# Kernel tuning notes

Hardware: AMD Instinct MI355X
Metric: run time of the kernel (lower is better)

The kernel has to match this reference:

```python
import jax, jax.numpy as jnp
import numpy as np

DT_REF = 1.0
EPS = 1e-5

def _ln(x, g, b):
    m = x.mean(-1, keepdims=True)
    v = ((x - m) ** 2).mean(-1, keepdims=True)
    return (x - m) * jax.lax.rsqrt(v + EPS) * g + b

def _conv(x, w):
    return jax.lax.conv_general_dilated(x, w, (1, 1), 'SAME', dimension_numbers=('NCHW', 'OIHW', 'NCHW'))

def _linscan(A, X):
    # h_t = A_t * h_{t-1} + X_t  via associative scan along axis=1 (time)
    def comb(c1, c2):
        a1, x1 = c1
        a2, x2 = c2
        return a1 * a2, x2 + a2 * x1
    return jax.lax.associative_scan(comb, (A, X), axis=1)[1]

def _forward(x_re, x_im, h_re, h_im, flux_re, flux_im, dt, gs_g, gs_b, wc_re, wc_im, bc_re, bc_im, metric, gt_g, gt_b, E_re, E_im, Einv_re, Einv_im, lam_flux, inj_re, inj_im, Wsrc_re, Wsrc_im, Wgate, bgate, lam_re, lam_im, Wg, W1, b1, W2, b2):
    B, T, D, H, W = x_re.shape
    x = jax.lax.complex(x_re, x_im)
    # ---- spatial: LayerNorm + Clifford (complex) conv scaled by Riemannian metric, residual ----
    xf = x.reshape(B * T, D, H, W)
    xr = jnp.concatenate([xf.real, xf.imag], axis=1)  # (N,2D,H,W)
    xn = _ln(xr.transpose(0, 2, 3, 1), gs_g, gs_b).transpose(0, 3, 1, 2)
    nr, ni = jnp.split(xn, 2, axis=1)
    o_re = (_conv(nr, wc_re) - _conv(ni, wc_im)) * metric + bc_re[None, :, None, None]
    o_im = (_conv(nr, wc_im) + _conv(ni, wc_re)) * metric + bc_im[None, :, None, None]
    x = (xf + jax.lax.complex(o_re, o_im)).reshape(B, T, D, H, W)
    # ---- eigenbasis encode ----
    E = jax.lax.complex(E_re, E_im)
    x_eigen = jnp.einsum('btdhw,de->bthwe', x, E)  # (B,T,H,W,D)
    x_mean = x_eigen.mean(axis=(2, 3))  # (B,T,D)
    dt_exp = jnp.broadcast_to(dt[None, :], (B, T))
    # ---- flux tracker: linear recurrence over T via pscan + carry-in correction ----
    A_flux = jnp.exp(-jax.nn.softplus(lam_flux)[None, None] * dt_exp[..., None] / DT_REF)  # (B,T,D) real
    X_flux = x_mean * jax.lax.complex(inj_re, inj_im)[None, None]
    flux_seq = _linscan(A_flux.astype(X_flux.dtype), X_flux)
    decay_cum = jnp.cumprod(A_flux, axis=1)
    flux_seq = flux_seq + jax.lax.complex(flux_re, flux_im)[:, None] * decay_cum
    source = jnp.einsum('btd,de->bte', flux_seq, jax.lax.complex(Wsrc_re, Wsrc_im))
    gate = jax.nn.sigmoid(flux_seq.real @ Wgate + bgate)  # (B,T,D) real in (0,1)
    g = gate[:, :, None, None, :]
    forcing = x_eigen * g + source[:, :, None, None, :] * (1.0 - g)
    # ---- ZOH transition operators ----
    lam = jax.lax.complex(-jax.nn.softplus(lam_re), lam_im)  # (D,) stable eigenvalues
    op_decay = jnp.exp(lam[None, None] * dt_exp[..., None])  # (B,T,D) complex
    op_forcing = (op_decay - 1.0) / lam
    u_t = forcing * op_forcing[:, :, None, None, :]
    h_prev = jax.lax.complex(h_re, h_im).reshape(B, H, W, D)
    u_t = u_t.at[:, 0].add(h_prev * op_decay[:, 0][:, None, None, :])
    A_full = jnp.broadcast_to(op_decay[:, :, None, None, :], u_t.shape)
    u_out = _linscan(A_full, u_t)  # state scan over T, independent per (b,h,w)
    # ---- decode + temporal LayerNorm + soft-MoE FFN residual ----
    x_dec = jnp.einsum('bthwe,ed->btdhw', u_out, jax.lax.complex(Einv_re, Einv_im))
    xr2 = jnp.concatenate([x_dec.real, x_dec.imag], axis=2).reshape(B * T, 2 * D, H, W)
    xn2 = _ln(xr2.transpose(0, 2, 3, 1), gt_g, gt_b)  # (N,H,W,2D)
    gates = jax.nn.softmax(xn2 @ Wg, axis=-1)  # (N,H,W,E)
    delta = jnp.zeros_like(xn2)
    for e in range(Wg.shape[-1]):  # small fixed expert count
        hdn = jax.nn.gelu(xn2 @ W1[e] + b1[e])
        delta = delta + gates[..., e:e + 1] * (hdn @ W2[e] + b2[e])
    y = xn2 + delta
    y_re, y_im = jnp.split(y, 2, axis=-1)
    x_out = jax.lax.complex(y_re, y_im).transpose(0, 3, 1, 2).reshape(B, T, D, H, W)
    z = x + x_out
    return jnp.concatenate([z.real, z.imag], axis=2)  # (B,T,2D,H,W) real view of complex out

def setup_inputs():
    B, T, D, H, W, E, F = 2, 16, 64, 48, 48, 4, 256
    key = jax.random.key(0)
    ks = jax.random.split(key, 32)
    n = lambda i, shape, s=1.0: jax.random.normal(ks[i], shape, dtype=jnp.float32) * s
    return {
        'x_re': n(0, (B, T, D, H, W)), 'x_im': n(1, (B, T, D, H, W)),
        'h_re': n(2, (B * H * W, 1, D)), 'h_im': n(3, (B * H * W, 1, D)),
        'flux_re': n(4, (B, D)), 'flux_im': n(5, (B, D)),
        'dt': jax.random.uniform(ks[6], (T,), dtype=jnp.float32, minval=0.1, maxval=1.0),
        'gs_g': jnp.ones((2 * D,), jnp.float32), 'gs_b': jnp.zeros((2 * D,), jnp.float32),
        'wc_re': n(7, (D, D, 3, 3), 0.02), 'wc_im': n(8, (D, D, 3, 3), 0.02),
        'bc_re': jnp.zeros((D,), jnp.float32), 'bc_im': jnp.zeros((D,), jnp.float32),
        'metric': jnp.ones((H, W), jnp.float32) + n(9, (H, W), 0.01),
        'gt_g': jnp.ones((2 * D,), jnp.float32), 'gt_b': jnp.zeros((2 * D,), jnp.float32),
        'E_re': n(10, (D, D), 0.125), 'E_im': n(11, (D, D), 0.125),
        'Einv_re': n(12, (D, D), 0.125), 'Einv_im': n(13, (D, D), 0.125),
        'lam_flux': n(14, (D,), 0.5),
        'inj_re': n(15, (D,), 0.1), 'inj_im': n(16, (D,), 0.1),
        'Wsrc_re': n(17, (D, D), 0.125), 'Wsrc_im': n(18, (D, D), 0.125),
        'Wgate': n(19, (D, D), 0.125), 'bgate': jnp.zeros((D,), jnp.float32),
        'lam_re': n(20, (D,), 0.5), 'lam_im': n(21, (D,), 0.5),
        'Wg': n(22, (2 * D, E), 0.1),
        'W1': n(23, (E, 2 * D, F), 0.06), 'b1': jnp.zeros((E, F), jnp.float32),
        'W2': n(24, (E, F, 2 * D), 0.04), 'b2': jnp.zeros((E, 2 * D), jnp.float32),
    }

def reference(x_re, x_im, h_re, h_im, flux_re, flux_im, dt, gs_g, gs_b, wc_re, wc_im, bc_re, bc_im, metric, gt_g, gt_b, E_re, E_im, Einv_re, Einv_im, lam_flux, inj_re, inj_im, Wsrc_re, Wsrc_im, Wgate, bgate, lam_re, lam_im, Wg, W1, b1, W2, b2):
    return _forward(x_re, x_im, h_re, h_im, flux_re, flux_im, dt, gs_g, gs_b, wc_re, wc_im, bc_re, bc_im, metric, gt_g, gt_b, E_re, E_im, Einv_re, Einv_im, lam_flux, inj_re, inj_im, Wsrc_re, Wsrc_im, Wgate, bgate, lam_re, lam_im, Wg, W1, b1, W2, b2)
```

## Files before the change

### kernel.cpp

```cpp
#include <hip/hip_runtime.h>
#include <hip/hip_bf16.h>
#include <math.h>

#define NBT 32
#define BB 2
#define TT 16
#define DD 64
#define CC 128
#define HH 48
#define WW2 48
#define HW 2304
#define NEXP 4
#define FF 256
#define EPS 1e-5f
#define PADROWS 2432

typedef __attribute__((ext_vector_type(8))) short bf16x8;
typedef __attribute__((ext_vector_type(4))) float f32x4;
typedef __attribute__((ext_vector_type(4))) unsigned int uint4v;
typedef __attribute__((ext_vector_type(2))) unsigned int uint2v;

static __device__ __forceinline__ unsigned short f2bf(float v) {
  __hip_bfloat16 h = __float2bfloat16(v);
  return *(unsigned short*)&h;
}

#define GLOAD_LDS16(gsrc, ldst) \
  __builtin_amdgcn_global_load_lds((const __attribute__((address_space(1))) unsigned int*)(gsrc), \
                                   (__attribute__((address_space(3))) unsigned int*)(ldst), 16, 0, 0)

__global__ void k_prep(unsigned int* __restrict__ xnb_u, float* __restrict__ xm,
                       const float* __restrict__ wc_re, const float* __restrict__ wc_im,
                       unsigned short* __restrict__ Wt,
                       const float* __restrict__ W1, const float* __restrict__ W2,
                       unsigned short* __restrict__ W1t, unsigned short* __restrict__ W2t,
                       const float* __restrict__ Einv_re, const float* __restrict__ Einv_im,
                       unsigned short* __restrict__ Bdt) {
  int blk = blockIdx.x;
  if (blk < 1024) {
    int u = blk * 256 + threadIdx.x;
    if (u < 4096) xm[u] = 0.f;
    if (u >= 32 * 128 * 64) return;
    int img = u >> 13;
    int rem = u & 8191;
    int row = rem >> 6;
    int cu  = rem & 63;
    int prow = row < 64 ? row : row + 2304;
    xnb_u[((size_t)img * PADROWS + prow) * 64 + cu] = 0u;
  } else if (blk < 1600) {
    int idx = (blk - 1024) * 256 + threadIdx.x;
    int tap = idx / 16384;
    int rem = idx & 16383;
    int cout = rem >> 7, cin = rem & 127;
    float v;
    if (cout < 64) {
      if (cin < 64) v =  wc_re[((size_t)cout * 64 + cin) * 9 + tap];
      else          v = -wc_im[((size_t)cout * 64 + (cin - 64)) * 9 + tap];
    } else {
      int o = cout - 64;
      if (cin < 64) v =  wc_im[((size_t)o * 64 + cin) * 9 + tap];
      else          v =  wc_re[((size_t)o * 64 + (cin - 64)) * 9 + tap];
    }
    Wt[idx] = f2bf(v);
  } else if (blk < 2112) {
    int idx = (blk - 1600) * 256 + threadIdx.x;
    {
      int e = idx >> 15, rem = idx & 32767, j = rem >> 7, k = rem & 127;
      float v = W1[((size_t)e * 128 + k) * 256 + j];
      int sw = ((((k >> 3) ^ (j & 7)) << 3) | (k & 7));
      W1t[(size_t)e * 32768 + j * 128 + sw] = f2bf(v);
    }
    {
      int e = idx >> 15, rem = idx & 32767, c = rem >> 8, k2 = rem & 255;
      float v = W2[((size_t)e * 256 + k2) * 128 + c];
      int sw = ((((k2 >> 3) ^ (c & 7)) << 3) | (k2 & 7));
      W2t[(size_t)e * 32768 + c * 256 + sw] = f2bf(v);
    }
  } else {
    int idx = (blk - 2112) * 256 + threadIdx.x;
    int j = idx >> 7, k = idx & 127;
    float v;
    if (j < 64) {
      if (k < 64) v =  Einv_re[k * 64 + j];
      else        v = -Einv_im[(k - 64) * 64 + j];
    } else {
      int d = j - 64;
      if (k < 64) v =  Einv_im[k * 64 + d];
      else        v =  Einv_re[(k - 64) * 64 + d];
    }
    int sw = ((((k >> 3) ^ (j & 7)) << 3) | (k & 7));
    Bdt[j * 128 + sw] = f2bf(v);
  }
}

__global__ void k_ln1(const float* __restrict__ x_re, const float* __restrict__ x_im,
                      const float* __restrict__ g, const float* __restrict__ b,
                      unsigned short* __restrict__ xnb) {
  int n = blockIdx.x / 36;
  int hw0 = (blockIdx.x % 36) * 64;
  __shared__ float ls[64][129];
  __shared__ float part_s[4][64], part_q[4][64];
  __shared__ float mean_s[64], rstd_s[64];
  int tid = threadIdx.x;
  for (int i = tid; i < 64 * 128; i += 256) {
    int d = i >> 6, p = i & 63;
    float v = (d < DD) ? x_re[((size_t)n * DD + d) * HW + hw0 + p]
                       : x_im[((size_t)n * DD + (d - DD)) * HW + hw0 + p];
    ls[p][d] = v;
  }
  __syncthreads();
  {
    int p = tid & 63, q = tid >> 6;
    float s = 0.f, ss = 0.f;
    for (int c = q * 32; c < q * 32 + 32; c++) { float v = ls[p][c]; s += v; ss += v * v; }
    part_s[q][p] = s; part_q[q][p] = ss;
  }
  __syncthreads();
  if (tid < 64) {
    float s = part_s[0][tid] + part_s[1][tid] + part_s[2][tid] + part_s[3][tid];
    float ss = part_q[0][tid] + part_q[1][tid] + part_q[2][tid] + part_q[3][tid];
    float m = s * (1.f / CC);
    float var = ss * (1.f / CC) - m * m;
    mean_s[tid] = m; rstd_s[tid] = rsqrtf(var + EPS);
  }
  __syncthreads();
  for (int i = tid; i < 64 * 128; i += 256) {
    int p = i >> 7, c = i & 127;
    float v = (ls[p][c] - mean_s[p]) * rstd_s[p] * g[c] + b[c];
    xnb[(((size_t)n * PADROWS) + 64 + hw0 + p) * 128 + c] = f2bf(v);
  }
}

#define TM 128
#define AROWS 226

__global__ __launch_bounds__(512, 1) void k_conv(
    const unsigned short* __restrict__ xnb,
    const unsigned short* __restrict__ Wt,
    const float* __restrict__ bc_re, const float* __restrict__ bc_im,
    const float* __restrict__ metric,
    const float* __restrict__ x_re, const float* __restrict__ x_im,
    float* __restrict__ xp) {
  __shared__ unsigned short As[AROWS * 128];
  __shared__ unsigned short Bs[2][128 * 128];
  int n = blockIdx.x / 18;
  int tile = blockIdx.x % 18;
  int hw0 = tile * TM;
  int tid = threadIdx.x;
  int lane = tid & 63, wv = tid >> 6;
  int wvp = wv >> 1, wvc = wv & 1;
  int r16 = lane & 15, kgrp = lane >> 4;

  const unsigned short* xbase = xnb + ((size_t)n * PADROWS + 64 + hw0 - 49) * 128;
  for (int i = tid; i < AROWS * 16; i += 512) {
    int row = i >> 4, ch = i & 15;
    GLOAD_LDS16(xbase + (size_t)row * 128 + ((ch ^ (row & 7)) << 3), &As[i * 8]);
  }
  {
    #pragma unroll
    for (int it = 0; it < 4; it++) {
      int i = it * 512 + tid;
      int row = i >> 4, ch = i & 15;
      GLOAD_LDS16(Wt + (size_t)row * 128 + ((ch ^ (row & 7)) << 3), &Bs[0][i * 8]);
    }
  }

  f32x4 acc[2][4];
  #pragma unroll
  for (int am = 0; am < 2; am++)
    #pragma unroll
    for (int n0 = 0; n0 < 4; n0++) acc[am][n0] = (f32x4){0.f, 0.f, 0.f, 0.f};

  int w0 = (hw0 + wvp * 32 + r16) % 48;
  int w1 = (hw0 + wvp * 32 + 16 + r16) % 48;

  __syncthreads();

  for (int tap = 0; tap < 9; tap++) {
    int cur = tap & 1;
    if (tap < 8) {
      const unsigned short* wbase = Wt + (size_t)(tap + 1) * 16384;
      #pragma unroll
      for (int it = 0; it < 4; it++) {
        int i = it * 512 + tid;
        int row = i >> 4, ch = i & 15;
        GLOAD_LDS16(wbase + (size_t)row * 128 + ((ch ^ (row & 7)) << 3), &Bs[cur ^ 1][i * 8]);
      }
    }
    int ky = tap / 3, kx = tap % 3;
    int delta = (ky - 1) * 48 + (kx - 1);
    bool v0 = (unsigned)(w0 + kx - 1) < 48u;
    bool v1 = (unsigned)(w1 + kx - 1) < 48u;
    int lp0 = wvp * 32 + r16 + delta + 49;
    int lp1 = lp0 + 16;
    __builtin_amdgcn_s_setprio(1);
    #pragma unroll
    for (int k0 = 0; k0 < 4; k0++) {
      bf16x8 a0 = {0,0,0,0,0,0,0,0}, a1 = {0,0,0,0,0,0,0,0};
      if (v0) a0 = *(const bf16x8*)(As + lp0 * 128 + (((k0 * 4 + kgrp) ^ (lp0 & 7)) << 3));
      if (v1) a1 = *(const bf16x8*)(As + lp1 * 128 + (((k0 * 4 + kgrp) ^ (lp1 & 7)) << 3));
      #pragma unroll
      for (int n0 = 0; n0 < 4; n0++) {
        int brow = wvc * 64 + n0 * 16 + r16;
        bf16x8 b = *(const bf16x8*)(&Bs[cur][brow * 128 + (((k0 * 4 + kgrp) ^ (brow & 7)) << 3)]);
        acc[0][n0] = __builtin_amdgcn_mfma_f32_16x16x32_bf16(a0, b, acc[0][n0], 0, 0, 0);
        acc[1][n0] = __builtin_amdgcn_mfma_f32_16x16x32_bf16(a1, b, acc[1][n0], 0, 0, 0);
      }
    }
    __builtin_amdgcn_s_setprio(0);
    __syncthreads();
  }

  #pragma unroll
  for (int am = 0; am < 2; am++) {
    int prow0 = wvp * 32 + am * 16 + kgrp * 4;
    int pix0 = hw0 + prow0;
    f32x4 mets = *(const f32x4*)(metric + pix0);
    #pragma unroll
    for (int n0 = 0; n0 < 4; n0++) {
      int col = wvc * 64 + n0 * 16 + r16;
      float bias = (col < DD) ? bc_re[col] : bc_im[col - DD];
      const float* xsrc = (col < DD) ? (x_re + ((size_t)n * DD + col) * HW)
                                     : (x_im + ((size_t)n * DD + (col - DD)) * HW);
      f32x4 xres = *(const f32x4*)(xsrc + pix0);
      #pragma unroll
      for (int j = 0; j < 4; j++) {
        float v = acc[am][n0][j] * mets[j] + bias + xres[j];
        xp[((size_t)n * HW + pix0 + j) * 128 + col] = v;
      }
    }
  }
}

__global__ __launch_bounds__(256, 2) void k_eigen(
    const float* __restrict__ xp,
    const float* __restrict__ E_re, const float* __restrict__ E_im,
    float* __restrict__ eg_re, float* __restrict__ eg_im,
    float* __restrict__ xm_re, float* __restrict__ xm_im) {
  __shared__ float Xs[64 * 128];
  __shared__ float Ers[4096], Eis[4096];
  int tid = threadIdx.x;
  int pos0 = blockIdx.x * 64;
  int n = blockIdx.x / 36;
  for (int i = tid; i < 4096; i += 256) { Ers[i] = E_re[i]; Eis[i] = E_im[i]; }
  const float* xb = xp + (size_t)pos0 * 128;
  #pragma unroll
  for (int it = 0; it < 8; it++) {
    int ci = it * 256 + tid;
    int p = ci >> 5, c4 = ci & 31;
    f32x4 v = *(const f32x4*)(xb + (size_t)ci * 4);
    *(f32x4*)&Xs[p * 128 + ((c4 ^ (p & 7)) << 2)] = v;
  }
  __syncthreads();
  int egq = tid & 15, pg = tid >> 4;
  int e0 = egq * 4, swz = pg & 7;
  f32x4 acr[4], aci[4];
  #pragma unroll
  for (int i = 0; i < 4; i++) { acr[i] = (f32x4){0.f,0.f,0.f,0.f}; aci[i] = (f32x4){0.f,0.f,0.f,0.f}; }
  for (int d4 = 0; d4 < 16; d4++) {
    f32x4 xr[4], xi[4];
    #pragma unroll
    for (int i = 0; i < 4; i++) {
      int p = pg + 16 * i;
      xr[i] = *(const f32x4*)&Xs[p * 128 + ((d4 ^ swz) << 2)];
      xi[i] = *(const f32x4*)&Xs[p * 128 + (((d4 + 16) ^ swz) << 2)];
    }
    #pragma unroll
    for (int j = 0; j < 4; j++) {
      int d = d4 * 4 + j;
      f32x4 er = *(const f32x4*)&Ers[d * 64 + e0];
      f32x4 ei = *(const f32x4*)&Eis[d * 64 + e0];
      #pragma unroll
      for (int i = 0; i < 4; i++) {
        acr[i] += xr[i][j] * er - xi[i][j] * ei;
        aci[i] += xr[i][j] * ei + xi[i][j] * er;
      }
    }
  }
  #pragma unroll
  for (int i = 0; i < 4; i++) {
    size_t p = (size_t)(pos0 + pg + 16 * i);
    *(f32x4*)&eg_re[p * 64 + e0] = acr[i];
    *(f32x4*)&eg_im[p * 64 + e0] = aci[i];
  }
  __syncthreads();
  float* red = (float*)Xs;
  f32x4 psr = acr[0] + acr[1] + acr[2] + acr[3];
  f32x4 psi = aci[0] + aci[1] + aci[2] + aci[3];
  *(f32x4*)&red[pg * 64 + e0] = psr;
  *(f32x4*)&red[1024 + pg * 64 + e0] = psi;
  __syncthreads();
  if (tid < 128) {
    int e = tid & 63, which = tid >> 6;
    const float* rb = red + which * 1024;
    float s = 0.f;
    #pragma unroll
    for (int p = 0; p < 16; p++) s += rb[p * 64 + e];
    float* dst = which ? xm_im : xm_re;
    atomicAdd(&dst[n * DD + e], s * (1.f / HW));
  }
}

__global__ void k_seq1(const float* __restrict__ xm_re, const float* __restrict__ xm_im,
                       const float* __restrict__ dt, const float* __restrict__ lam_flux,
                       const float* __restrict__ inj_re, const float* __restrict__ inj_im,
                       const float* __restrict__ flux_re0, const float* __restrict__ flux_im0,
                       float* __restrict__ frg, float* __restrict__ fig) {
  int b = blockIdx.x;
  int e = threadIdx.x;
  float lx = lam_flux[e];
  float sp = lx > 20.f ? lx : log1pf(expf(lx));
  float f_r = flux_re0[b * DD + e], f_i = flux_im0[b * DD + e];
  float ij_r = inj_re[e], ij_i = inj_im[e];
  for (int t = 0; t < TT; t++) {
    float A = expf(-sp * dt[t]);
    int bt = b * TT + t;
    float xr = xm_re[bt * DD + e], xi = xm_im[bt * DD + e];
    f_r = A * f_r + (xr * ij_r - xi * ij_i);
    f_i = A * f_i + (xr * ij_i + xi * ij_r);
    frg[bt * DD + e] = f_r; fig[bt * DD + e] = f_i;
  }
}

__global__ void k_seq2(const float* __restrict__ frg, const float* __restrict__ fig,
                       const float* __restrict__ dt,
                       const float* __restrict__ Wsrc_re, const float* __restrict__ Wsrc_im,
                       const float* __restrict__ Wgate, const float* __restrict__ bgate,
                       const float* __restrict__ lam_re, const float* __restrict__ lam_im,
                       float* __restrict__ gate, float* __restrict__ src_re, float* __restrict__ src_im,
                       float* __restrict__ od_re, float* __restrict__ od_im,
                       float* __restrict__ of_re, float* __restrict__ of_im) {
  int bt = blockIdx.x;
  int t = bt % TT;
  int e = threadIdx.x;
  __shared__ float fr[DD], fi[DD];
  fr[e] = frg[bt * DD + e];
  fi[e] = fig[bt * DD + e];
  __syncthreads();
  float sr = 0.f, si = 0.f, gl = bgate[e];
  for (int d2 = 0; d2 < DD; d2++) {
    float r = fr[d2], im = fi[d2];
    float wr = Wsrc_re[d2 * DD + e], wi = Wsrc_im[d2 * DD + e];
    sr += r * wr - im * wi;
    si += r * wi + im * wr;
    gl += r * Wgate[d2 * DD + e];
  }
  src_re[bt * DD + e] = sr; src_im[bt * DD + e] = si;
  gate[bt * DD + e] = 1.f / (1.f + expf(-gl));
  float lre = lam_re[e];
  float lr_v = -(lre > 20.f ? lre : log1pf(expf(lre)));
  float li_v = lam_im[e];
  float den = lr_v * lr_v + li_v * li_v;
  float dtv = dt[t];
  float mag = expf(lr_v * dtv);
  float odr = mag * cosf(li_v * dtv);
  float odi = mag * sinf(li_v * dtv);
  od_re[bt * DD + e] = odr; od_im[bt * DD + e] = odi;
  of_re[bt * DD + e] = ((odr - 1.f) * lr_v + odi * li_v) / den;
  of_im[bt * DD + e] = (odi * lr_v - (odr - 1.f) * li_v) / den;
}

__global__ void k_uscan(float* __restrict__ eg_re, float* __restrict__ eg_im,
                        const float* __restrict__ gate,
                        const float* __restrict__ src_re, const float* __restrict__ src_im,
                        const float* __restrict__ od_re, const float* __restrict__ od_im,
                        const float* __restrict__ of_re, const float* __restrict__ of_im,
                        const float* __restrict__ h_re, const float* __restrict__ h_im) {
  size_t gid = (size_t)blockIdx.x * 256 + threadIdx.x;
  int e = (int)(gid & 63);
  size_t rem = gid >> 6;
  int hw = (int)(rem % HW);
  int b = (int)(rem / HW);
  float u_r = 0.f, u_i = 0.f;
  for (int t = 0; t < TT; t++) {
    int bt = b * TT + t;
    size_t idx = ((size_t)bt * HW + hw) * DD + e;
    float g = gate[bt * DD + e];
    float fr2 = eg_re[idx] * g + src_re[bt * DD + e] * (1.f - g);
    float fi2 = eg_im[idx] * g + src_im[bt * DD + e] * (1.f - g);
    float ofr = of_re[bt * DD + e], ofi = of_im[bt * DD + e];
    float ut_r = fr2 * ofr - fi2 * ofi;
    float ut_i = fr2 * ofi + fi2 * ofr;
    float odr = od_re[bt * DD + e], odi = od_im[bt * DD + e];
    if (t == 0) {
      size_t hidx = ((size_t)b * HW + hw) * DD + e;
      float hr = h_re[hidx], hi = h_im[hidx];
      ut_r += hr * odr - hi * odi;
      ut_i += hr * odi + hi * odr;
    }
    float nu_r = odr * u_r - odi * u_i + ut_r;
    float nu_i = odr * u_i + odi * u_r + ut_i;
    u_r = nu_r; u_i = nu_i;
    eg_re[idx] = u_r; eg_im[idx] = u_i;
  }
}

__global__ __launch_bounds__(256, 2) void k_dmoe(
    const float* u_re, const float* u_im,
    const unsigned short* __restrict__ Bdt,
    const float* __restrict__ Wg,
    float* __restrict__ gates,
    const float* __restrict__ xp,
    const unsigned short* __restrict__ W1t, const unsigned short* __restrict__ W2t,
    const float* __restrict__ b1, const float* __restrict__ b2,
    const float* __restrict__ gt_g, const float* __restrict__ gt_b,
    float* __restrict__ out) {
  __shared__ __attribute__((aligned(16))) unsigned char smem[81920];
  int tid = threadIdx.x;
  int blk = blockIdx.x;
  int n = blk / 36;
  int hw0 = (blk % 36) * 64;
  size_t pos0 = (size_t)blk * 64;
  int lane = tid & 63, w = tid >> 6, wm = w >> 1, wn = w & 1;
  int r16 = lane & 15, kgrp = lane >> 4;

  {
    unsigned short* BdL = (unsigned short*)smem;
    unsigned short* Au  = (unsigned short*)(smem + 32768);
    #pragma unroll
    for (int it = 0; it < 8; it++)
      GLOAD_LDS16(Bdt + (size_t)(it * 256 + tid) * 8, &BdL[(it * 256 + tid) * 8]);
    #pragma unroll
    for (int it = 0; it < 8; it++) {
      int ci = it * 256 + tid;
      int p = ci >> 5, c4 = ci & 31;
      f32x4 v;
      if (c4 < 16) v = *(const f32x4*)(u_re + (size_t)(pos0 + p) * 64 + c4 * 4);
      else         v = *(const f32x4*)(u_im + (size_t)(pos0 + p) * 64 + (c4 - 16) * 4);
      unsigned int lo = (unsigned int)f2bf(v[0]) | ((unsigned int)f2bf(v[1]) << 16);
      unsigned int hi = (unsigned int)f2bf(v[2]) | ((unsigned int)f2bf(v[3]) << 16);
      int chunk = c4 >> 1, sub = (c4 & 1) * 4;
      *(uint2v*)&Au[p * 128 + ((chunk ^ (p & 7)) << 3) + sub] = (uint2v){lo, hi};
    }
    __syncthreads();
    f32x4 accD[2][4];
    #pragma unroll
    for (int mt = 0; mt < 2; mt++)
      #pragma unroll
      for (int nt = 0; nt < 4; nt++) accD[mt][nt] = (f32x4){0.f, 0.f, 0.f, 0.f};
    #pragma unroll
    for (int ks = 0; ks < 4; ks++) {
      int kc = ks * 4 + kgrp;
      bf16x8 a[2], bb[4];
      #pragma unroll
      for (int mt = 0; mt < 2; mt++) {
        int r = wm * 32 + mt * 16 + r16;
        a[mt] = *(const bf16x8*)&Au[r * 128 + ((kc ^ (r & 7)) << 3)];
      }
      #pragma unroll
      for (int nt = 0; nt < 4; nt++) {
        int j = wn * 64 + nt * 16 + r16;
        bb[nt] = *(const bf16x8*)&BdL[j * 128 + ((kc ^ (j & 7)) << 3)];
      }
      #pragma unroll
      for (int mt = 0; mt < 2; mt++)
        #pragma unroll
        for (int nt = 0; nt < 4; nt++)
          accD[mt][nt] = __builtin_amdgcn_mfma_f32_16x16x32_bf16(a[mt], bb[nt], accD[mt][nt], 0, 0, 0);
    }
    __syncthreads();
    float* DsD = (float*)smem;
    #pragma unroll
    for (int mt = 0; mt < 2; mt++) {
      int row0 = wm * 32 + mt * 16 + kgrp * 4;
      #pragma unroll
      for (int nt = 0; nt < 4; nt++) {
        int c = wn * 64 + nt * 16 + r16;
        #pragma unroll
        for (int jj = 0; jj < 4; jj++)
          DsD[(row0 + jj) * 128 + c] = accD[mt][nt][jj];
      }
    }
    __syncthreads();
    float* Yl = (float*)(smem + 32768);
    unsigned short* Xb = (unsigned short*)(smem + 65536);
    int egq = tid & 15, pg = tid >> 4;
    int d0 = egq * 4, swz = pg & 7;
    f32x4 gg0 = *(const f32x4*)(gt_g + d0);
    f32x4 gb0 = *(const f32x4*)(gt_b + d0);
    f32x4 gg1 = *(const f32x4*)(gt_g + 64 + d0);
    f32x4 gb1 = *(const f32x4*)(gt_b + 64 + d0);
    f32x4 wgr[4], wgi[4];
    #pragma unroll
    for (int j = 0; j < 4; j++) {
      wgr[j] = *(const f32x4*)&Wg[(d0 + j) * 4];
      wgi[j] = *(const f32x4*)&Wg[(64 + d0 + j) * 4];
    }
    int cre = ((d0 >> 3) ^ swz) << 3;
    int cim = (((64 + d0) >> 3) ^ swz) << 3;
    int off47 = d0 & 7;
    #pragma unroll
    for (int i = 0; i < 4; i++) {
      int p = pg + 16 * i;
      size_t pos = pos0 + p;
      f32x4 acr = *(const f32x4*)&DsD[p * 128 + d0];
      f32x4 aci = *(const f32x4*)&DsD[p * 128 + 64 + d0];
      float s = acr[0] + acr[1] + acr[2] + acr[3]
              + aci[0] + aci[1] + aci[2] + aci[3];
      float q = acr[0]*acr[0] + acr[1]*acr[1] + acr[2]*acr[2] + acr[3]*acr[3]
              + aci[0]*aci[0] + aci[1]*aci[1] + aci[2]*aci[2] + aci[3]*aci[3];
      #pragma unroll
      for (int off = 8; off >= 1; off >>= 1) {
        s += __shfl_xor(s, off);
        q += __shfl_xor(q, off);
      }
      float mean = s * (1.f / CC);
      float rstd = rsqrtf(q * (1.f / CC) - mean * mean + EPS);
      f32x4 lnr = (acr - mean) * rstd * gg0 + gb0;
      f32x4 lni = (aci - mean) * rstd * gg1 + gb1;
      *(f32x4*)&Yl[p * 128 + d0] = lnr;
      *(f32x4*)&Yl[p * 128 + 64 + d0] = lni;
      f32x4 p4 = lnr[0]*wgr[0] + lnr[1]*wgr[1] + lnr[2]*wgr[2] + lnr[3]*wgr[3]
               + lni[0]*wgi[0] + lni[1]*wgi[1] + lni[2]*wgi[2] + lni[3]*wgi[3];
      float p0 = p4[0], p1 = p4[1], p2 = p4[2], p3 = p4[3];
      #pragma unroll
      for (int off = 8; off >= 1; off >>= 1) {
        p0 += __shfl_xor(p0, off); p1 += __shfl_xor(p1, off);
        p2 += __shfl_xor(p2, off); p3 += __shfl_xor(p3, off);
      }
      if (egq == 0) {
        float m = fmaxf(fmaxf(p0, p1), fmaxf(p2, p3));
        float e0v = __expf(p0 - m), e1v = __expf(p1 - m), e2v = __expf(p2 - m), e3v = __expf(p3 - m);
        float inv = 1.f / (e0v + e1v + e2v + e3v);
        f32x4 g4 = {e0v * inv, e1v * inv, e2v * inv, e3v * inv};
        *(f32x4*)(gates + pos * 4) = g4;
      }
      unsigned int r0 = (unsigned int)f2bf(lnr[0]) | ((unsigned int)f2bf(lnr[1]) << 16);
      unsigned int r1 = (unsigned int)f2bf(lnr[2]) | ((unsigned int)f2bf(lnr[3]) << 16);
      unsigned int i0 = (unsigned int)f2bf(lni[0]) | ((unsigned int)f2bf(lni[1]) << 16);
      unsigned int i1 = (unsigned int)f2bf(lni[2]) | ((unsigned int)f2bf(lni[3]) << 16);
      *(uint2v*)&Xb[p * 128 + cre + off47] = (uint2v){r0, r1};
      *(uint2v*)&Xb[p * 128 + cim + off47] = (uint2v){i0, i1};
    }
  }
  __syncthreads();

  unsigned short* W1s = (unsigned short*)smem;
  unsigned short* W2s = (unsigned short*)(smem + 32768);
  unsigned short* Hs  = (unsigned short*)(smem + 65536);
  float* Ds = (float*)smem;
  f32x4 acc2[2][4];
  {
    const float* YlF = (const float*)(smem + 32768);
    #pragma unroll
    for (int mt = 0; mt < 2; mt++) {
      int row0 = wm * 32 + mt * 16 + kgrp * 4;
      #pragma unroll
      for (int nt = 0; nt < 4; nt++) {
        int c = wn * 64 + nt * 16 + r16;
        #pragma unroll
        for (int jj = 0; jj < 4; jj++)
          acc2[mt][nt][jj] = YlF[(row0 + jj) * 128 + c];
      }
    }
  }
  bf16x8 xa[2][4];
  {
    const unsigned short* Xb = (const unsigned short*)(smem + 65536);
    #pragma unroll
    for (int pt = 0; pt < 2; pt++) {
      int r = wm * 32 + pt * 16 + r16;
      #pragma unroll
      for (int ks = 0; ks < 4; ks++) {
        int kc = ks * 4 + kgrp;
        xa[pt][ks] = *(const bf16x8*)&Xb[r * 128 + ((kc ^ (r & 7)) << 3)];
      }
    }
  }
  __syncthreads();
  {
    #pragma unroll
    for (int it = 0; it < 8; it++)
      GLOAD_LDS16(W1t + (size_t)(it * 256 + tid) * 8, &W1s[(it * 256 + tid) * 8]);
  }
  __syncthreads();

  const float c1 = -2.3022084f;
  const float c2 = -0.10294372f;

  for (int s = 0; s < 8; s++) {
    int e = s >> 1, h = s & 1;
    float grp[2];
    #pragma unroll
    for (int pt = 0; pt < 2; pt++)
      grp[pt] = gates[(pos0 + wm * 32 + pt * 16 + r16) * 4 + e];
    f32x4 b1p[4];
    #pragma unroll
    for (int ft = 0; ft < 4; ft++)
      b1p[ft] = *(const f32x4*)&b1[e * 256 + h * 128 + wn * 64 + ft * 16 + kgrp * 4];
    {
      const unsigned short* w2src = W2t + (size_t)e * 32768 + (size_t)h * 128;
      #pragma unroll
      for (int it = 0; it < 8; it++) {
        int i = it * 256 + tid;
        int c = i >> 4, j = i & 15;
        GLOAD_LDS16(w2src + (size_t)c * 256 + j * 8, &W2s[i * 8]);
      }
    }
    f32x4 acc1[4][2];
    #pragma unroll
    for (int ft = 0; ft < 4; ft++)
      #pragma unroll
      for (int pt = 0; pt < 2; pt++) acc1[ft][pt] = (f32x4){0.f, 0.f, 0.f, 0.f};
    __builtin_amdgcn_s_setprio(1);
    #pragma unroll
    for (int ks = 0; ks < 4; ks++) {
      int kc = ks * 4 + kgrp;
      bf16x8 wf[4];
      #pragma unroll
      for (int ft = 0; ft < 4; ft++) {
        int fr = wn * 64 + ft * 16 + r16;
        wf[ft] = *(const bf16x8*)&W1s[fr * 128 + ((kc ^ (fr & 7)) << 3)];
      }
      #pragma unroll
      for (int ft = 0; ft < 4; ft++)
        #pragma unroll
        for (int pt = 0; pt < 2; pt++)
          acc1[ft][pt] = __builtin_amdgcn_mfma_f32_16x16x32_bf16(wf[ft], xa[pt][ks], acc1[ft][pt], 0, 0, 0);
    }
    __builtin_amdgcn_s_setprio(0);
    #pragma unroll
    for (int ft = 0; ft < 4; ft++) {
      int f0 = wn * 64 + ft * 16 + kgrp * 4;
      int chunk = f0 >> 3, sub = f0 & 7;
      #pragma unroll
      for (int pt = 0; pt < 2; pt++) {
        int pl = wm * 32 + pt * 16 + r16;
        float gr = grp[pt];
        unsigned short hb[4];
        #pragma unroll
        for (int jj = 0; jj < 4; jj++) {
          float x = acc1[ft][pt][jj] + b1p[ft][jj];
          float z = x * (c1 + c2 * x * x);
          float t = __builtin_amdgcn_exp2f(z);
          hb[jj] = f2bf(x * gr * __builtin_amdgcn_rcpf(1.f + t));
        }
        unsigned int lo = (unsigned int)hb[0] | ((unsigned int)hb[1] << 16);
        unsigned int hi = (unsigned int)hb[2] | ((unsigned int)hb[3] << 16);
        *(uint2v*)&Hs[pl * 128 + ((chunk ^ (pl & 7)) << 3) + sub] = (uint2v){lo, hi};
      }
    }
    __syncthreads();
    if (s < 7) {
      int sn = s + 1;
      const unsigned short* w1src = W1t + (size_t)(sn >> 1) * 32768 + (size_t)(sn & 1) * 16384;
      #pragma unroll
      for (int it = 0; it < 8; it++)
        GLOAD_LDS16(w1src + (size_t)(it * 256 + tid) * 8, &W1s[(it * 256 + tid) * 8]);
    }
    __builtin_amdgcn_s_setprio(1);
    #pragma unroll
    for (int ks = 0; ks < 4; ks++) {
      int kc = ks * 4 + kgrp;
      bf16x8 a[2], bb[4];
      #pragma unroll
      for (int mt = 0; mt < 2; mt++) {
        int r = wm * 32 + mt * 16 + r16;
        a[mt] = *(const bf16x8*)&Hs[r * 128 + ((kc ^ (r & 7)) << 3)];
      }
      #pragma unroll
      for (int nt = 0; nt < 4; nt++) {
        int c = wn * 64 + nt * 16 + r16;
        bb[nt] = *(const bf16x8*)&W2s[c * 128 + ((kc ^ (c & 7)) << 3)];
      }
      #pragma unroll
      for (int mt = 0; mt < 2; mt++)
        #pragma unroll
        for (int nt = 0; nt < 4; nt++)
          acc2[mt][nt] = __builtin_amdgcn_mfma_f32_16x16x32_bf16(a[mt], bb[nt], acc2[mt][nt], 0, 0, 0);
    }
    __builtin_amdgcn_s_setprio(0);
    __syncthreads();
  }

  #pragma unroll
  for (int mt = 0; mt < 2; mt++) {
    int row0 = wm * 32 + mt * 16 + kgrp * 4;
    #pragma unroll
    for (int nt = 0; nt < 4; nt++) {
      int c = wn * 64 + nt * 16 + r16;
      #pragma unroll
      for (int jj = 0; jj < 4; jj++)
        Ds[(row0 + jj) * 129 + c] = acc2[mt][nt][jj];
    }
  }
  __syncthreads();
  #pragma unroll
  for (int it = 0; it < 8; it++) {
    int qi = it * 256 + tid;
    int p = qi >> 5, cq = (qi & 31) << 2;
    size_t pos = pos0 + p;
    f32x4 xpv = *(const f32x4*)&xp[pos * 128 + cq];
    f32x4 g4  = *(const f32x4*)&gates[pos * 4];
    f32x4 bt0 = *(const f32x4*)&b2[0 * CC + cq];
    f32x4 bt1 = *(const f32x4*)&b2[1 * CC + cq];
    f32x4 bt2 = *(const f32x4*)&b2[2 * CC + cq];
    f32x4 bt3 = *(const f32x4*)&b2[3 * CC + cq];
    int base = p * 129 + cq;
    #pragma unroll
    for (int j = 0; j < 4; j++) {
      float bterm = g4[0] * bt0[j] + g4[1] * bt1[j] + g4[2] * bt2[j] + g4[3] * bt3[j];
      Ds[base + j] = xpv[j] + Ds[base + j] + bterm;
    }
  }
  __syncthreads();
  {
    int p = tid & 63;
    int cg = tid >> 6;
    const float* Drow = Ds + p * 129;
    size_t obase = ((size_t)n * CC) * HW + hw0 + p;
    #pragma unroll
    for (int i = 0; i < 32; i++) {
      int c = i * 4 + cg;
      out[obase + (size_t)c * HW] = Drow[c];
    }
  }
}

extern "C" void kernel_launch(void* const* d_in, const int* in_sizes, int n_in,
                              void* d_out, int out_size, void* d_ws, size_t ws_size,
                              hipStream_t stream) {
  const float* x_re   = (const float*)d_in[0];
  const float* x_im   = (const float*)d_in[1];
  const float* h_re   = (const float*)d_in[2];
  const float* h_im   = (const float*)d_in[3];
  const float* flux_re= (const float*)d_in[4];
  const float* flux_im= (const float*)d_in[5];
  const float* dt     = (const float*)d_in[6];
  const float* gs_g   = (const float*)d_in[7];
  const float* gs_b   = (const float*)d_in[8];
  const float* wc_re  = (const float*)d_in[9];
  const float* wc_im  = (const float*)d_in[10];
  const float* bc_re  = (const float*)d_in[11];
  const float* bc_im  = (const float*)d_in[12];
  const float* metric = (const float*)d_in[13];
  const float* gt_g   = (const float*)d_in[14];
  const float* gt_b   = (const float*)d_in[15];
  const float* E_re   = (const float*)d_in[16];
  const float* E_im   = (const float*)d_in[17];
  const float* Einv_re= (const float*)d_in[18];
  const float* Einv_im= (const float*)d_in[19];
  const float* lam_flux=(const float*)d_in[20];
  const float* inj_re = (const float*)d_in[21];
  const float* inj_im = (const float*)d_in[22];
  const float* Wsrc_re= (const float*)d_in[23];
  const float* Wsrc_im= (const float*)d_in[24];
  const float* Wgate  = (const float*)d_in[25];
  const float* bgate  = (const float*)d_in[26];
  const float* lam_re = (const float*)d_in[27];
  const float* lam_im = (const float*)d_in[28];
  const float* Wg     = (const float*)d_in[29];
  const float* W1     = (const float*)d_in[30];
  const float* b1     = (const float*)d_in[31];
  const float* W2     = (const float*)d_in[32];
  const float* b2     = (const float*)d_in[33];

  float* ws = (float*)d_ws;
  const size_t SZ_FULL = (size_t)NBT * HW * CC;
  const size_t SZ_HALF = (size_t)NBT * HW * DD;
  float* xp    = ws;
  float* eg_re = xp + SZ_FULL;
  float* eg_im = eg_re + SZ_HALF;
  float* xr2   = eg_im + SZ_HALF;
  unsigned short* xnb = (unsigned short*)xr2;
  unsigned short* Wt  = (unsigned short*)(xr2 + 5000000);
  float* smalls = xr2 + SZ_FULL;
  float* xm_re = smalls;
  float* xm_im = xm_re + 2048;
  float* gatep = xm_im + 2048;
  float* src_re= gatep + 2048;
  float* src_im= src_re + 2048;
  float* od_re = src_im + 2048;
  float* od_im = od_re + 2048;
  float* of_re = od_im + 2048;
  float* of_im = of_re + 2048;
  float* gates = of_im + 2048;
  unsigned short* W1t = (unsigned short*)(gates + (size_t)NBT * HW * 4);
  unsigned short* W2t = W1t + 131072;
  float* frg = (float*)(W2t + 131072);
  float* fig = frg + 2048;
  unsigned short* Bdt = (unsigned short*)(fig + 2048);

  hipLaunchKernelGGL(k_prep, dim3(2176), dim3(256), 0, stream,
                     (unsigned int*)xnb, xm_re, wc_re, wc_im, Wt, W1, W2, W1t, W2t,
                     Einv_re, Einv_im, Bdt);
  hipLaunchKernelGGL(k_ln1, dim3(NBT * 36), dim3(256), 0, stream, x_re, x_im, gs_g, gs_b, xnb);
  hipLaunchKernelGGL(k_conv, dim3(NBT * 18), dim3(512), 0, stream,
                     xnb, Wt, bc_re, bc_im, metric, x_re, x_im, xp);
  hipLaunchKernelGGL(k_eigen, dim3(1152), dim3(256), 0, stream,
                     xp, E_re, E_im, eg_re, eg_im, xm_re, xm_im);
  hipLaunchKernelGGL(k_seq1, dim3(BB), dim3(DD), 0, stream,
                     xm_re, xm_im, dt, lam_flux, inj_re, inj_im, flux_re, flux_im, frg, fig);
  hipLaunchKernelGGL(k_seq2, dim3(NBT), dim3(DD), 0, stream,
                     frg, fig, dt, Wsrc_re, Wsrc_im, Wgate, bgate, lam_re, lam_im,
                     gatep, src_re, src_im, od_re, od_im, of_re, of_im);
  hipLaunchKernelGGL(k_uscan, dim3(1152), dim3(256), 0, stream,
                     eg_re, eg_im, gatep, src_re, src_im, od_re, od_im, of_re, of_im, h_re, h_im);
  hipLaunchKernelGGL(k_dmoe, dim3(1152), dim3(256), 0, stream,
                     eg_re, eg_im, Bdt, Wg,
                     gates, xp, W1t, W2t, b1, b2, gt_g, gt_b,
                     (float*)d_out);
}
```

Before: 228.5 us.

## Compute eigenbasis projection with bf16 MFMA using a pre-packed complex weight matrix

The complex einsum in k_eigen moves from fp32 scalar FMAs to bf16 MFMA 16x16x32. k_prep gains a block range that packs E_re/E_im into a swizzled 128x128 real-block bf16 matrix, which k_eigen loads into LDS with global_load_lds. The xp tile is converted to bf16 before the multiply. Results are staged through LDS for the stores and the mean reduction. This cuts ALU time in the kernel but lowers the eigen projection to bf16 precision and enlarges the shared-memory footprint.

```diff
diff --git a/kernel.cpp b/kernel.cpp
--- a/kernel.cpp
+++ b/kernel.cpp
@@ -35,7 +35,9 @@
                        const float* __restrict__ W1, const float* __restrict__ W2,
                        unsigned short* __restrict__ W1t, unsigned short* __restrict__ W2t,
                        const float* __restrict__ Einv_re, const float* __restrict__ Einv_im,
-                       unsigned short* __restrict__ Bdt) {
+                       unsigned short* __restrict__ Bdt,
+                       const float* __restrict__ E_re, const float* __restrict__ E_im,
+                       unsigned short* __restrict__ Bet) {
   int blk = blockIdx.x;
   if (blk < 1024) {
     int u = blk * 256 + threadIdx.x;
@@ -76,7 +78,7 @@
       int sw = ((((k2 >> 3) ^ (c & 7)) << 3) | (k2 & 7));
       W2t[(size_t)e * 32768 + c * 256 + sw] = f2bf(v);
     }
-  } else {
+  } else if (blk < 2176) {
     int idx = (blk - 2112) * 256 + threadIdx.x;
     int j = idx >> 7, k = idx & 127;
     float v;
@@ -90,6 +92,20 @@
     }
     int sw = ((((k >> 3) ^ (j & 7)) << 3) | (k & 7));
     Bdt[j * 128 + sw] = f2bf(v);
+  } else {
+    int idx = (blk - 2176) * 256 + threadIdx.x;
+    int j = idx >> 7, k = idx & 127;
+    float v;
+    if (j < 64) {
+      if (k < 64) v =  E_re[k * 64 + j];
+      else        v = -E_im[(k - 64) * 64 + j];
+    } else {
+      int d = j - 64;
+      if (k < 64) v =  E_im[k * 64 + d];
+      else        v =  E_re[(k - 64) * 64 + d];
+    }
+    int sw = ((((k >> 3) ^ (j & 7)) << 3) | (k & 7));
+    Bet[j * 128 + sw] = f2bf(v);
   }
 }
 
@@ -234,59 +250,86 @@
 
 __global__ __launch_bounds__(256, 2) void k_eigen(
     const float* __restrict__ xp,
-    const float* __restrict__ E_re, const float* __restrict__ E_im,
+    const unsigned short* __restrict__ Bet,
     float* __restrict__ eg_re, float* __restrict__ eg_im,
     float* __restrict__ xm_re, float* __restrict__ xm_im) {
-  __shared__ float Xs[64 * 128];
-  __shared__ float Ers[4096], Eis[4096];
+  __shared__ __attribute__((aligned(16))) unsigned char smem[81920];
   int tid = threadIdx.x;
-  int pos0 = blockIdx.x * 64;
-  int n = blockIdx.x / 36;
-  for (int i = tid; i < 4096; i += 256) { Ers[i] = E_re[i]; Eis[i] = E_im[i]; }
-  const float* xb = xp + (size_t)pos0 * 128;
+  int blk = blockIdx.x;
+  int n = blk / 36;
+  size_t pos0 = (size_t)blk * 64;
+  int lane = tid & 63, w = tid >> 6, wm = w >> 1, wn = w & 1;
+  int r16 = lane & 15, kgrp = lane >> 4;
+
+  unsigned short* BeL = (unsigned short*)smem;
+  unsigned short* Axp = (unsigned short*)(smem + 32768);
+  #pragma unroll
+  for (int it = 0; it < 8; it++)
+    GLOAD_LDS16(Bet + (size_t)(it * 256 + tid) * 8, &BeL[(it * 256 + tid) * 8]);
   #pragma unroll
   for (int it = 0; it < 8; it++) {
     int ci = it * 256 + tid;
     int p = ci >> 5, c4 = ci & 31;
-    f32x4 v = *(const f32x4*)(xb + (size_t)ci * 4);
-    *(f32x4*)&Xs[p * 128 + ((c4 ^ (p & 7)) << 2)] = v;
-  }
-  __syncthreads();
+    f32x4 v = *(const f32x4*)(xp + (pos0 + p) * 128 + c4 * 4);
+    unsigned int lo = (unsigned int)f2bf(v[0]) | ((unsigned int)f2bf(v[1]) << 16);
+    unsigned int hi = (unsigned int)f2bf(v[2]) | ((unsigned int)f2bf(v[3]) << 16);
+    int chunk = c4 >> 1, sub = (c4 & 1) * 4;
+    *(uint2v*)&Axp[p * 128 + ((chunk ^ (p & 7)) << 3) + sub] = (uint2v){lo, hi};
+  }
+  __syncthreads();
+  f32x4 accD[2][4];
+  #pragma unroll
+  for (int mt = 0; mt < 2; mt++)
+    #pragma unroll
+    for (int nt = 0; nt < 4; nt++) accD[mt][nt] = (f32x4){0.f, 0.f, 0.f, 0.f};
+  #pragma unroll
+  for (int ks = 0; ks < 4; ks++) {
+    int kc = ks * 4 + kgrp;
+    bf16x8 a[2], bb[4];
+    #pragma unroll
+    for (int mt = 0; mt < 2; mt++) {
+      int r = wm * 32 + mt * 16 + r16;
+      a[mt] = *(const bf16x8*)&Axp[r * 128 + ((kc ^ (r & 7)) << 3)];
+    }
+    #pragma unroll
+    for (int nt = 0; nt < 4; nt++) {
+      int j = wn * 64 + nt * 16 + r16;
+      bb[nt] = *(const bf16x8*)&BeL[j * 128 + ((kc ^ (j & 7)) << 3)];
+    }
+    #pragma unroll
+    for (int mt = 0; mt < 2; mt++)
+      #pragma unroll
+      for (int nt = 0; nt < 4; nt++)
+        accD[mt][nt] = __builtin_amdgcn_mfma_f32_16x16x32_bf16(a[mt], bb[nt], accD[mt][nt], 0, 0, 0);
+  }
+  __syncthreads();
+  float* DsD = (float*)smem;
+  #pragma unroll
+  for (int mt = 0; mt < 2; mt++) {
+    int row0 = wm * 32 + mt * 16 + kgrp * 4;
+    #pragma unroll
+    for (int nt = 0; nt < 4; nt++) {
+      int c = wn * 64 + nt * 16 + r16;
+      #pragma unroll
+      for (int jj = 0; jj < 4; jj++)
+        DsD[(row0 + jj) * 128 + c] = accD[mt][nt][jj];
+    }
+  }
+  __syncthreads();
+  float* red = (float*)(smem + 32768);
   int egq = tid & 15, pg = tid >> 4;
-  int e0 = egq * 4, swz = pg & 7;
-  f32x4 acr[4], aci[4];
-  #pragma unroll
-  for (int i = 0; i < 4; i++) { acr[i] = (f32x4){0.f,0.f,0.f,0.f}; aci[i] = (f32x4){0.f,0.f,0.f,0.f}; }
-  for (int d4 = 0; d4 < 16; d4++) {
-    f32x4 xr[4], xi[4];
-    #pragma unroll
-    for (int i = 0; i < 4; i++) {
-      int p = pg + 16 * i;
-      xr[i] = *(const f32x4*)&Xs[p * 128 + ((d4 ^ swz) << 2)];
-      xi[i] = *(const f32x4*)&Xs[p * 128 + (((d4 + 16) ^ swz) << 2)];
-    }
-    #pragma unroll
-    for (int j = 0; j < 4; j++) {
-      int d = d4 * 4 + j;
-      f32x4 er = *(const f32x4*)&Ers[d * 64 + e0];
-      f32x4 ei = *(const f32x4*)&Eis[d * 64 + e0];
-      #pragma unroll
-      for (int i = 0; i < 4; i++) {
-        acr[i] += xr[i][j] * er - xi[i][j] * ei;
-        aci[i] += xr[i][j] * ei + xi[i][j] * er;
-      }
-    }
-  }
+  int e0 = egq * 4;
+  f32x4 psr = (f32x4){0.f,0.f,0.f,0.f}, psi = (f32x4){0.f,0.f,0.f,0.f};
   #pragma unroll
   for (int i = 0; i < 4; i++) {
-    size_t p = (size_t)(pos0 + pg + 16 * i);
-    *(f32x4*)&eg_re[p * 64 + e0] = acr[i];
-    *(f32x4*)&eg_im[p * 64 + e0] = aci[i];
-  }
-  __syncthreads();
-  float* red = (float*)Xs;
-  f32x4 psr = acr[0] + acr[1] + acr[2] + acr[3];
-  f32x4 psi = aci[0] + aci[1] + aci[2] + aci[3];
+    int p = pg + 16 * i;
+    size_t pos = pos0 + p;
+    f32x4 ar = *(const f32x4*)&DsD[p * 128 + e0];
+    f32x4 ai = *(const f32x4*)&DsD[p * 128 + 64 + e0];
+    *(f32x4*)&eg_re[pos * 64 + e0] = ar;
+    *(f32x4*)&eg_im[pos * 64 + e0] = ai;
+    psr += ar; psi += ai;
+  }
   *(f32x4*)&red[pg * 64 + e0] = psr;
   *(f32x4*)&red[1024 + pg * 64 + e0] = psi;
   __syncthreads();
@@ -780,15 +823,16 @@
   float* frg = (float*)(W2t + 131072);
   float* fig = frg + 2048;
   unsigned short* Bdt = (unsigned short*)(fig + 2048);
-
-  hipLaunchKernelGGL(k_prep, dim3(2176), dim3(256), 0, stream,
+  unsigned short* Bet = Bdt + 16384;
+
+  hipLaunchKernelGGL(k_prep, dim3(2240), dim3(256), 0, stream,
                      (unsigned int*)xnb, xm_re, wc_re, wc_im, Wt, W1, W2, W1t, W2t,
-                     Einv_re, Einv_im, Bdt);
+                     Einv_re, Einv_im, Bdt, E_re, E_im, Bet);
   hipLaunchKernelGGL(k_ln1, dim3(NBT * 36), dim3(256), 0, stream, x_re, x_im, gs_g, gs_b, xnb);
   hipLaunchKernelGGL(k_conv, dim3(NBT * 18), dim3(512), 0, stream,
                      xnb, Wt, bc_re, bc_im, metric, x_re, x_im, xp);
   hipLaunchKernelGGL(k_eigen, dim3(1152), dim3(256), 0, stream,
-                     xp, E_re, E_im, eg_re, eg_im, xm_re, xm_im);
+                     xp, Bet, eg_re, eg_im, xm_re, xm_im);
   hipLaunchKernelGGL(k_seq1, dim3(BB), dim3(DD), 0, stream,
                      xm_re, xm_im, dt, lam_flux, inj_re, inj_im, flux_re, flux_im, frg, fig);
   hipLaunchKernelGGL(k_seq2, dim3(NBT), dim3(DD), 0, stream,
```

After: 203.9 us. 1.12x faster.
